# Kernel tuning notes

Hardware: AMD Instinct MI355X
Metric: run time of the kernel (lower is better)

The kernel has to match this reference:

```python
import jax, jax.numpy as jnp
import numpy as np
from jax import lax

B = 8; DIM = 256; NH = 8; PATCH = 8; WS = 28; STRIDE = 8; PAD = 14; ORF = 2.0; IMG = 448


def conv2d(x, w, stride, pad, groups=1):
    return lax.conv_general_dilated(
        x, w, (stride, stride), [(pad, pad), (pad, pad)],
        dimension_numbers=('NCHW', 'OIHW', 'NCHW'), feature_group_count=groups)


def ln_ch(x, g, b):
    # LayerNormProxy: LayerNorm over channel dim of NCHW
    m = jnp.mean(x, 1, keepdims=True)
    v = jnp.mean((x - m) ** 2, 1, keepdims=True)
    return (x - m) * lax.rsqrt(v + 1e-5) * g[None, :, None, None] + b[None, :, None, None]


def bilinear_sample(x, grid):
    # x: (N,C,H,W); grid: (N,Hg,Wg,2) in (x,y) order, [-1,1], align_corners=True, zeros padding
    N, C, H, W = x.shape
    gx = (grid[..., 0] + 1.0) * 0.5 * (W - 1)
    gy = (grid[..., 1] + 1.0) * 0.5 * (H - 1)
    x0 = jnp.floor(gx); y0 = jnp.floor(gy)
    x1 = x0 + 1.0; y1 = y0 + 1.0
    wx1 = gx - x0; wx0 = 1.0 - wx1
    wy1 = gy - y0; wy0 = 1.0 - wy1
    xf = x.reshape(N, C, H * W)

    def corner(ix, iy, w):
        valid = (ix >= 0) & (ix <= W - 1) & (iy >= 0) & (iy <= H - 1)
        ii = (jnp.clip(iy, 0, H - 1) * W + jnp.clip(ix, 0, W - 1)).astype(jnp.int32).reshape(N, -1)
        vals = jax.vmap(lambda f, i: f[:, i])(xf, ii)  # (N,C,Hg*Wg)
        return vals * (w * valid).reshape(N, 1, -1)

    out = (corner(x0, y0, wx0 * wy0) + corner(x1, y0, wx1 * wy0)
           + corner(x0, y1, wx0 * wy1) + corner(x1, y1, wx1 * wy1))
    return out.reshape(N, C, grid.shape[1], grid.shape[2])


def setup_inputs() -> dict:
    key = jax.random.key(0)
    ks = jax.random.split(key, 12)
    s = 0.02
    CG = 64
    return {
        'x': jax.random.normal(ks[0], (B, 3, IMG, IMG), jnp.float32),
        'patch_w': jax.random.normal(ks[1], (DIM, 3, PATCH, PATCH), jnp.float32) * s,
        'patch_b': jnp.zeros((DIM,), jnp.float32),
        'ln1_g': jnp.ones((DIM,), jnp.float32),
        'ln1_b': jnp.zeros((DIM,), jnp.float32),
        'wq': jax.random.normal(ks[2], (DIM, DIM), jnp.float32) * s,
        'bq': jnp.zeros((DIM,), jnp.float32),
        'wk': jax.random.normal(ks[3], (DIM, DIM), jnp.float32) * s,
        'bk': jnp.zeros((DIM,), jnp.float32),
        'wv': jax.random.normal(ks[4], (DIM, DIM), jnp.float32) * s,
        'bv': jnp.zeros((DIM,), jnp.float32),
        'wo': jax.random.normal(ks[5], (DIM, DIM), jnp.float32) * s,
        'bo': jnp.zeros((DIM,), jnp.float32),
        'off_dw_w': jax.random.normal(ks[6], (CG, 1, WS, WS), jnp.float32) * s,
        'off_dw_b': jnp.zeros((CG,), jnp.float32),
        'off_ln_g': jnp.ones((CG,), jnp.float32),
        'off_ln_b': jnp.zeros((CG,), jnp.float32),
        'off_pw_w': jax.random.normal(ks[7], (2, CG), jnp.float32) * s,
        'rpe_w1': jax.random.normal(ks[8], (32, 2), jnp.float32) * 0.1,
        'rpe_b1': jnp.zeros((32,), jnp.float32),
        'rpe_w2': jax.random.normal(ks[9], (2, 32), jnp.float32) * 0.1,
    }


def reference(x, patch_w, patch_b, ln1_g, ln1_b, wq, bq, wk, bk, wv, bv, wo, bo,
              off_dw_w, off_dw_b, off_ln_g, off_ln_b, off_pw_w, rpe_w1, rpe_b1, rpe_w2):
    Bn = x.shape[0]
    # patch embedding: Conv2d(3, dim, patch, patch) + LayerNormProxy
    feat = conv2d(x, patch_w, PATCH, 0) + patch_b[None, :, None, None]
    feat = ln_ch(feat, ln1_g, ln1_b)
    H, W = feat.shape[2], feat.shape[3]  # 56, 56
    G = (H // WS) * (W // WS)            # 4 groups
    CG = DIM // G; GH = NH // G; HC = DIM // NH
    # q projection (1x1 conv)
    q = jnp.einsum('oc,bchw->bohw', wq, feat) + bq[None, :, None, None]
    # offset network on per-group query features
    q_off = q.reshape(Bn * G, CG, H, W)
    off = conv2d(q_off, off_dw_w, STRIDE, PAD, groups=CG) + off_dw_b[None, :, None, None]
    off = jax.nn.gelu(ln_ch(off, off_ln_g, off_ln_b), approximate=False)
    off = jnp.einsum('oc,bchw->bohw', off_pw_w, off)   # (B*G, 2, Hk, Wk)
    Hk, Wk = off.shape[2], off.shape[3]
    ns = Hk * Wk
    rng = jnp.array([1.0 / (Hk - 1), 1.0 / (Wk - 1)], off.dtype).reshape(1, 2, 1, 1)
    offset = jnp.tanh(off) * rng * ORF
    offset = jnp.transpose(offset, (0, 2, 3, 1))  # (B*G, Hk, Wk, 2) in (y, x)
    # reference points, normalized to ~[-1, 1]
    ry = jnp.linspace(0.5, Hk - 0.5, Hk) / (Hk - 1) * 2.0 - 1.0
    rx = jnp.linspace(0.5, Wk - 0.5, Wk) / (Wk - 1) * 2.0 - 1.0
    ref = jnp.stack(jnp.meshgrid(ry, rx, indexing='ij'), -1)  # (Hk, Wk, 2)
    ref = jnp.broadcast_to(ref[None], (Bn * G, Hk, Wk, 2))
    pos = offset + ref
    # deformable sampling (grid expects (x, y) order)
    xs = bilinear_sample(feat.reshape(Bn * G, CG, H, W), pos[..., ::-1])  # (B*G, CG, Hk, Wk)
    xs = xs.reshape(Bn, DIM, ns)
    k = jnp.einsum('oc,bcn->bon', wk, xs) + bk[None, :, None]
    v = jnp.einsum('oc,bcn->bon', wv, xs) + bv[None, :, None]
    qh = q.reshape(Bn * NH, HC, H * W)
    kh = k.reshape(Bn * NH, HC, ns)
    vh = v.reshape(Bn * NH, HC, ns)
    attn = jnp.einsum('bcm,bcn->bmn', qh, kh) * (HC ** -0.5)  # (B*NH, HW, ns)
    # log-CPB relative position bias
    qy = jnp.linspace(0.0, float(H), H) / (H - 1) * 2.0 - 1.0
    qx = jnp.linspace(0.0, float(W), W) / (W - 1) * 2.0 - 1.0
    qg = jnp.stack(jnp.meshgrid(qy, qx, indexing='ij'), -1).reshape(H * W, 2)
    disp = (qg[None, :, None, :] - pos.reshape(Bn * G, ns, 2)[:, None, :, :]) * 4.0
    disp = jnp.sign(disp) * jnp.log2(jnp.abs(disp) + 1.0) / 3.0  # /log2(8)
    bias = jax.nn.relu(jnp.einsum('bmnc,hc->bmnh', disp, rpe_w1) + rpe_b1)
    bias = jnp.einsum('bmnh,oh->bmno', bias, rpe_w2)  # (B*G, HW, ns, GH)
    attn = attn + jnp.transpose(bias, (0, 3, 1, 2)).reshape(Bn * NH, H * W, ns)
    attn = jax.nn.softmax(attn, axis=-1)
    out = jnp.einsum('bmn,bcn->bcm', attn, vh).reshape(Bn, DIM, H, W)
    y = jnp.einsum('oc,bchw->bohw', wo, out) + bo[None, :, None, None]
    return (y, pos.reshape(Bn, G, Hk, Wk, 2), ref.reshape(Bn, G, Hk, Wk, 2))
```

## Files before the change

kernel.cpp:

```cpp
#include <hip/hip_runtime.h>
#include <cstddef>


typedef short bf16x8 __attribute__((ext_vector_type(8)));
typedef float f32x4 __attribute__((ext_vector_type(4)));

static __device__ __forceinline__ ushort f2bf(float f) {
  union { float f; unsigned u; } v; v.f = f;
  unsigned r = v.u + 0x7fffu + ((v.u >> 16) & 1u);
  return (ushort)(r >> 16);
}
static __device__ __forceinline__ float bf2f(ushort u) {
  union { unsigned u; float f; } v; v.u = ((unsigned)u) << 16;
  return v.f;
}

#define OFF_FEATB 0u
#define OFF_QPK   3211264u
#define OFF_Q     6422528u
#define OFF_POS   12845056u
#define OFF_XS    12849152u
#define OFF_KPK   12980224u
#define OFF_VPK   13045760u
#define OFF_PWP   13111296u
#define OFF_WQP   13135872u
#define OFF_WOP   13168640u
#define OFF_WKT   13201408u
#define OFF_WVT   13266944u

__global__ __launch_bounds__(256) void k_xcvt(
    const float* __restrict__ x, ushort* __restrict__ xb) {
  const size_t i0 = ((size_t)blockIdx.x * 256 + threadIdx.x) * 8;
  float4 v0 = *(const float4*)(x + i0);
  float4 v1 = *(const float4*)(x + i0 + 4);
  bf16x8 o;
  o[0] = (short)f2bf(v0.x); o[1] = (short)f2bf(v0.y);
  o[2] = (short)f2bf(v0.z); o[3] = (short)f2bf(v0.w);
  o[4] = (short)f2bf(v1.x); o[5] = (short)f2bf(v1.y);
  o[6] = (short)f2bf(v1.z); o[7] = (short)f2bf(v1.w);
  *(bf16x8*)(xb + i0) = o;
}

__global__ __launch_bounds__(256) void k_pack(
    const float* __restrict__ pw, const float* __restrict__ wq,
    const float* __restrict__ wk, const float* __restrict__ wv,
    const float* __restrict__ wo, ushort* __restrict__ pwp,
    ushort* __restrict__ wqp, ushort* __restrict__ wop,
    float* __restrict__ wkT, float* __restrict__ wvT) {
  const int o = blockIdx.x, t = threadIdx.x, m = blockIdx.y;
  if (m == 0) {
    if (t < 192) pwp[((t >> 3) * 256 + o) * 8 + (t & 7)] = f2bf(pw[o * 192 + t]);
  } else if (m == 1) {
    wqp[((t >> 3) * 256 + o) * 8 + (t & 7)] = f2bf(wq[o * 256 + t]);
  } else if (m == 2) {
    wop[((t >> 3) * 256 + o) * 8 + (t & 7)] = f2bf(wo[o * 256 + t]);
  } else if (m == 3) {
    wkT[t * 256 + o] = wk[o * 256 + t];
  } else {
    wvT[t * 256 + o] = wv[o * 256 + t];
  }
}

__global__ __launch_bounds__(256) void k_patch_mfma(
    const ushort* __restrict__ xb, const ushort* __restrict__ pwp,
    const float* __restrict__ pb, const float* __restrict__ g1,
    const float* __restrict__ b1, ushort* __restrict__ featb) {
  __shared__ ushort Bs[2][8192];
  const int t = threadIdx.x;
  const int lane = t & 63, w = t >> 6;
  const int lr = lane & 15, kg = lane >> 4;
  const int m_base = blockIdx.x * 128 + w * 32;

  size_t abase[2];
#pragma unroll
  for (int mr = 0; mr < 2; mr++) {
    int mA = m_base + mr * 16 + lr;
    int bA = mA / 3136;
    int posA = mA - bA * 3136;
    int ohA = posA / 56;
    int owA = posA - ohA * 56;
    abase[mr] = (((size_t)bA * 3) * 448 + ohA * 8) * 448 + owA * 8;
  }

  f32x4 acc[2][16];
#pragma unroll
  for (int f = 0; f < 16; f++) {
    float bv = pb[f * 16 + lr];
    acc[0][f] = (f32x4){bv, bv, bv, bv};
    acc[1][f] = (f32x4){bv, bv, bv, bv};
  }

  bf16x8 st[4];
#pragma unroll
  for (int i = 0; i < 4; i++)
    st[i] = *(const bf16x8*)(pwp + i * 2048 + t * 8);
#pragma unroll
  for (int i = 0; i < 4; i++)
    *(bf16x8*)(&Bs[0][i * 2048 + t * 8]) = st[i];
  __syncthreads();
  int p = 0;
  for (int ks = 0; ks < 6; ks++) {
    if (ks < 5) {
#pragma unroll
      for (int i = 0; i < 4; i++)
        st[i] = *(const bf16x8*)(pwp + (ks + 1) * 8192 + i * 2048 + t * 8);
    }
    const int k8 = ks * 4 + kg;
    const int ci = k8 >> 3, ii = k8 & 7;
    bf16x8 a0 = *(const bf16x8*)(xb + abase[0] + (size_t)ci * 200704 + ii * 448);
    bf16x8 a1 = *(const bf16x8*)(xb + abase[1] + (size_t)ci * 200704 + ii * 448);
    const ushort* bsl = &Bs[p][kg * 2048];
#pragma unroll
    for (int f = 0; f < 16; f++) {
      bf16x8 bfr = *(const bf16x8*)(bsl + (f * 16 + lr) * 8);
      acc[0][f] = __builtin_amdgcn_mfma_f32_16x16x32_bf16(a0, bfr, acc[0][f], 0, 0, 0);
      acc[1][f] = __builtin_amdgcn_mfma_f32_16x16x32_bf16(a1, bfr, acc[1][f], 0, 0, 0);
    }
    __syncthreads();
    if (ks < 5) {
#pragma unroll
      for (int i = 0; i < 4; i++)
        *(bf16x8*)(&Bs[p ^ 1][i * 2048 + t * 8]) = st[i];
      __syncthreads();
      p ^= 1;
    }
  }

#pragma unroll
  for (int mr = 0; mr < 2; mr++) {
    float mean[4], rstd[4];
#pragma unroll
    for (int j = 0; j < 4; j++) {
      float s1 = 0.f, s2 = 0.f;
#pragma unroll
      for (int f = 0; f < 16; f++) { float v = acc[mr][f][j]; s1 += v; s2 += v * v; }
#pragma unroll
      for (int off = 8; off >= 1; off >>= 1) {
        s1 += __shfl_xor(s1, off);
        s2 += __shfl_xor(s2, off);
      }
      float mn = s1 * (1.f / 256.f);
      float var = s2 * (1.f / 256.f) - mn * mn;
      mean[j] = mn; rstd[j] = rsqrtf(var + 1e-5f);
    }
#pragma unroll
    for (int f = 0; f < 16; f++) {
      const int c = f * 16 + lr;
      const float gg = g1[c], bb = b1[c];
#pragma unroll
      for (int j = 0; j < 4; j++) {
        const int mo = m_base + mr * 16 + kg * 4 + j;
        float v = (acc[mr][f][j] - mean[j]) * rstd[j] * gg + bb;
        featb[(size_t)mo * 256 + c] = f2bf(v);
      }
    }
  }
}

__global__ __launch_bounds__(256) void k_gemm_mfma(
    const ushort* __restrict__ apk, const ushort* __restrict__ wp,
    const float* __restrict__ bias, float* __restrict__ out,
    ushort* __restrict__ opk) {
  __shared__ float smem[16448];
  ushort* Bs = (ushort*)smem;
  float* sA = smem;
  const int t = threadIdx.x;
  const int lane = t & 63, w = t >> 6;
  const int lr = lane & 15, kg = lane >> 4;
  const int m_base = blockIdx.x * 128 + w * 32;

  f32x4 acc[2][16];
#pragma unroll
  for (int f = 0; f < 16; f++) {
    float bv = bias[f * 16 + lr];
    acc[0][f] = (f32x4){bv, bv, bv, bv};
    acc[1][f] = (f32x4){bv, bv, bv, bv};
  }
  const ushort* a0p = apk + (size_t)(m_base + lr) * 256;
  const ushort* a1p = a0p + 16 * 256;

  bf16x8 st[4];
#pragma unroll
  for (int i = 0; i < 4; i++) st[i] = *(const bf16x8*)(wp + i * 2048 + t * 8);
#pragma unroll
  for (int i = 0; i < 4; i++) *(bf16x8*)(Bs + i * 2048 + t * 8) = st[i];
  __syncthreads();
  int p = 0;
  for (int ks = 0; ks < 8; ks++) {
    if (ks < 7) {
#pragma unroll
      for (int i = 0; i < 4; i++)
        st[i] = *(const bf16x8*)(wp + (ks + 1) * 8192 + i * 2048 + t * 8);
    }
    bf16x8 a0 = *(const bf16x8*)(a0p + ks * 32 + kg * 8);
    bf16x8 a1 = *(const bf16x8*)(a1p + ks * 32 + kg * 8);
    const ushort* bsl = Bs + p * 8192 + kg * 2048;
#pragma unroll
    for (int f = 0; f < 16; f++) {
      bf16x8 bfr = *(const bf16x8*)(bsl + (f * 16 + lr) * 8);
      acc[0][f] = __builtin_amdgcn_mfma_f32_16x16x32_bf16(a0, bfr, acc[0][f], 0, 0, 0);
      acc[1][f] = __builtin_amdgcn_mfma_f32_16x16x32_bf16(a1, bfr, acc[1][f], 0, 0, 0);
    }
    __syncthreads();
    if (ks < 7) {
#pragma unroll
      for (int i = 0; i < 4; i++)
        *(bf16x8*)(Bs + (p ^ 1) * 8192 + i * 2048 + t * 8) = st[i];
      __syncthreads();
      p ^= 1;
    }
  }
  __syncthreads();

#pragma unroll
  for (int h = 0; h < 2; h++) {
    if ((w >> 1) == h) {
      const int loc0 = (w & 1) * 32;
#pragma unroll
      for (int mr = 0; mr < 2; mr++)
#pragma unroll
        for (int f = 0; f < 16; f++)
#pragma unroll
          for (int j = 0; j < 4; j++)
            sA[(loc0 + mr * 16 + kg * 4 + j) * 257 + f * 16 + lr] = acc[mr][f][j];
    }
    __syncthreads();
    const int R0 = blockIdx.x * 128 + h * 64;
    const int bh = R0 / 3136;
    const int pos0 = R0 % 3136;
    {
      const int c = t;
      float* op = out + ((size_t)bh * 256 + c) * 3136 + pos0;
#pragma unroll
      for (int i4 = 0; i4 < 16; i4++) {
        float4 v;
        v.x = sA[(i4 * 4 + 0) * 257 + c];
        v.y = sA[(i4 * 4 + 1) * 257 + c];
        v.z = sA[(i4 * 4 + 2) * 257 + c];
        v.w = sA[(i4 * 4 + 3) * 257 + c];
        *(float4*)(op + i4 * 4) = v;
      }
    }
    if (opk) {
      const int mm = t & 63, cs = t >> 6;
      const int c0 = cs * 64;
#pragma unroll
      for (int jj = 0; jj < 8; jj++) {
        bf16x8 v8;
#pragma unroll
        for (int e = 0; e < 8; e++)
          v8[e] = (short)f2bf(sA[mm * 257 + c0 + jj * 8 + e]);
        *(bf16x8*)(opk + (size_t)(R0 + mm) * 256 + c0 + jj * 8) = v8;
      }
    }
    __syncthreads();
  }
}

__global__ __launch_bounds__(128) void k_offset_conv(
    const float* __restrict__ q, const float* __restrict__ dww,
    float* __restrict__ convo) {
  const int bg = blockIdx.y;
  const int wv = threadIdx.x >> 6;
  const int lane = threadIdx.x & 63;
  const int ch = blockIdx.x * 2 + wv;
  const int b = bg >> 2, g = bg & 3;

  __shared__ float pl[2][7072];
  float* P = pl[wv];
  for (int idx = lane; idx < 7072; idx += 64) P[idx] = 0.f;

  const float* qb = q + ((size_t)b * 256 + g * 64 + ch) * 3136;
  if (lane < 56) {
    for (int r = 0; r < 56; r++) {
      int hr = r + 14;
      P[hr * 84 + (lane + 14) + (hr >> 3)] = qb[r * 56 + lane];
    }
  }
  const int oh = lane >> 3, ow = lane & 7;
  const int chs = __builtin_amdgcn_readfirstlane(ch);
  const float* wr = dww + (size_t)chs * 784;
  float acc = 0.f;
  const int r0 = oh * 8, c0 = ow * 8;
  for (int i = 0; i < 28; i++) {
    int hr = r0 + i;
    const float* prow = P + hr * 84 + c0 + (hr >> 3);
    const float* wrr = wr + i * 28;
#pragma unroll
    for (int j = 0; j < 28; j++)
      acc = fmaf(prow[j], wrr[j], acc);
  }
  convo[bg * 4096 + lane * 64 + ch] = acc;
}

__global__ __launch_bounds__(256) void k_offset_post(
    const float* __restrict__ convo, const float* __restrict__ dwb,
    const float* __restrict__ lng, const float* __restrict__ lnb,
    const float* __restrict__ pww, float* __restrict__ pos_ws,
    float* __restrict__ out_pos, float* __restrict__ out_ref) {
  const int bg = blockIdx.y;
  const int wv = threadIdx.x >> 6;
  const int lane = threadIdx.x & 63;
  const int idx = blockIdx.x * 4 + wv;
  const int oh = idx >> 3, ow = idx & 7;

  float acc = convo[bg * 4096 + idx * 64 + lane] + dwb[lane];

  float s1 = acc, s2 = acc * acc;
#pragma unroll
  for (int off = 32; off >= 1; off >>= 1) {
    s1 += __shfl_xor(s1, off);
    s2 += __shfl_xor(s2, off);
  }
  float m = s1 * (1.f / 64.f);
  float var = s2 * (1.f / 64.f) - m * m;
  float val = (acc - m) * rsqrtf(var + 1e-5f) * lng[lane] + lnb[lane];
  val = 0.5f * val * (1.f + erff(val * 0.70710678118654752f));
  float p0 = pww[lane] * val, p1 = pww[64 + lane] * val;
#pragma unroll
  for (int off = 32; off >= 1; off >>= 1) {
    p0 += __shfl_xor(p0, off);
    p1 += __shfl_xor(p1, off);
  }
  if (lane == 0) {
    float offy = tanhf(p0) * (2.0f / 7.0f);
    float offx = tanhf(p1) * (2.0f / 7.0f);
    float ry = (0.5f + oh) * (2.0f / 7.0f) - 1.0f;
    float rx = (0.5f + ow) * (2.0f / 7.0f) - 1.0f;
    float py = offy + ry, px = offx + rx;
    int o = bg * 128 + idx * 2;
    pos_ws[o] = py;  pos_ws[o + 1] = px;
    out_pos[o] = py; out_pos[o + 1] = px;
    out_ref[o] = ry; out_ref[o + 1] = rx;
  }
}

__global__ __launch_bounds__(256) void k_sample_kv(
    const ushort* __restrict__ featb, const float* __restrict__ pos_ws,
    const float* __restrict__ wkT, const float* __restrict__ bk,
    const float* __restrict__ wvT, const float* __restrict__ bv,
    ushort* __restrict__ kpk, ushort* __restrict__ vpk) {
  const int b = blockIdx.y;
  const int n = blockIdx.x;
  const int t = threadIdx.x;
  const int g = t >> 6, lane = t & 63;
  const int bg = b * 4 + g;

  __shared__ float sxs[256];
  {
    float py = pos_ws[bg * 128 + n * 2];
    float px = pos_ws[bg * 128 + n * 2 + 1];
    float gx = (px + 1.f) * 27.5f;
    float gy = (py + 1.f) * 27.5f;
    float x0f = floorf(gx), y0f = floorf(gy);
    int x0 = (int)x0f, y0 = (int)y0f;
    float wx1 = gx - x0f, wx0 = 1.f - wx1;
    float wy1 = gy - y0f, wy0 = 1.f - wy1;
    const size_t mb = (size_t)b * 3136;
    const int cofs = g * 64 + lane;
    float acc = 0.f;
    if (x0 >= 0 && x0 <= 55 && y0 >= 0 && y0 <= 55)
      acc = fmaf(bf2f(featb[(mb + y0 * 56 + x0) * 256 + cofs]), wx0 * wy0, acc);
    if (x0 + 1 >= 0 && x0 + 1 <= 55 && y0 >= 0 && y0 <= 55)
      acc = fmaf(bf2f(featb[(mb + y0 * 56 + x0 + 1) * 256 + cofs]), wx1 * wy0, acc);
    if (x0 >= 0 && x0 <= 55 && y0 + 1 >= 0 && y0 + 1 <= 55)
      acc = fmaf(bf2f(featb[(mb + (y0 + 1) * 56 + x0) * 256 + cofs]), wx0 * wy1, acc);
    if (x0 + 1 >= 0 && x0 + 1 <= 55 && y0 + 1 >= 0 && y0 + 1 <= 55)
      acc = fmaf(bf2f(featb[(mb + (y0 + 1) * 56 + x0 + 1) * 256 + cofs]), wx1 * wy1, acc);
    sxs[g * 64 + lane] = acc;
  }
  __syncthreads();

  float ak = bk[t], av = bv[t];
  for (int c = 0; c < 256; c++) {
    float xv = sxs[c];
    ak = fmaf(wkT[c * 256 + t], xv, ak);
    av = fmaf(wvT[c * 256 + t], xv, av);
  }
  const int h = t >> 5, cc = t & 31;
  const size_t base = (size_t)(b * 8 + h) * 2048;
  kpk[base + (size_t)((cc >> 3) * 64 + n) * 8 + (cc & 7)] = f2bf(ak);
  vpk[base + (size_t)((n >> 3) * 32 + cc) * 8 + (n & 7)] = f2bf(av);
}

__global__ __launch_bounds__(256) void k_attn_mfma(
    const ushort* __restrict__ qpk, const ushort* __restrict__ kpk,
    const ushort* __restrict__ vpk, const float* __restrict__ pos_ws,
    const float* __restrict__ w1, const float* __restrict__ b1,
    const float* __restrict__ w2, ushort* __restrict__ attnpk) {
  const int bg = blockIdx.y;
  const int b = bg >> 2, g = bg & 3;
  const int m0 = blockIdx.x * 64;
  const int t = threadIdx.x;
  const int lane = t & 63, w = t >> 6;
  const int lr = lane & 15, kg = lane >> 4;

  __shared__ ushort Pbuf[4][16 * 88];
  __shared__ ushort outb[64 * 72];
  __shared__ float posl[128];
  __shared__ float4 rpe4[32];
  __shared__ float rpeB[32];

  if (t < 128) posl[t] = pos_ws[bg * 128 + t];
  if (t < 32) {
    rpe4[t] = make_float4(w1[t * 2], w1[t * 2 + 1], b1[t], w2[t]);
    rpeB[t] = w2[32 + t];
  }
  __syncthreads();

  float qgy[4], qgx[4];
#pragma unroll
  for (int j = 0; j < 4; j++) {
    int m = m0 + w * 16 + kg * 4 + j;
    int my = m / 56, mx = m % 56;
    qgy[j] = (float)my * (56.0f / 55.0f) * (2.0f / 55.0f) - 1.0f;
    qgx[j] = (float)mx * (56.0f / 55.0f) * (2.0f / 55.0f) - 1.0f;
  }
  float tyv[16], txv[16];
#pragma unroll
  for (int nf = 0; nf < 4; nf++) {
    int n = nf * 16 + lr;
    float py = posl[2 * n], px = posl[2 * n + 1];
#pragma unroll
    for (int j = 0; j < 4; j++) {
      float dy = (qgy[j] - py) * 4.f;
      float dx = (qgx[j] - px) * 4.f;
      tyv[nf * 4 + j] = copysignf(__log2f(fabsf(dy) + 1.f) * (1.f / 3.f), dy);
      txv[nf * 4 + j] = copysignf(__log2f(fabsf(dx) + 1.f) * (1.f / 3.f), dx);
    }
  }
  float bb0[16], bb1[16];
#pragma unroll
  for (int p = 0; p < 16; p++) { bb0[p] = 0.f; bb1[p] = 0.f; }
  for (int jj = 0; jj < 32; jj++) {
    float4 r = rpe4[jj];
    float wb = rpeB[jj];
#pragma unroll
    for (int p = 0; p < 16; p++) {
      float hv = fmaxf(fmaf(r.x, tyv[p], fmaf(r.y, txv[p], r.z)), 0.f);
      bb0[p] = fmaf(r.w, hv, bb0[p]);
      bb1[p] = fmaf(wb, hv, bb1[p]);
    }
  }

  const int mrow = m0 + w * 16 + lr;
  const float scale = 0.17677669529663687f;
  ushort* pb = Pbuf[w];

  f32x4 oacc[2][2];
#pragma unroll
  for (int gh = 0; gh < 2; gh++)
#pragma unroll
    for (int cf = 0; cf < 2; cf++) oacc[gh][cf] = (f32x4){0.f, 0.f, 0.f, 0.f};

#pragma unroll
  for (int gh = 0; gh < 2; gh++) {
    bf16x8 a = *(const bf16x8*)(qpk +
        ((size_t)(b * 3136 + mrow) * 256 + g * 64 + gh * 32 + kg * 8));
    const ushort* kbase = kpk + (size_t)(b * 8 + g * 2 + gh) * 2048;
    f32x4 s[4];
#pragma unroll
    for (int nf = 0; nf < 4; nf++) {
      bf16x8 bfr = *(const bf16x8*)(kbase + (size_t)(kg * 64 + nf * 16 + lr) * 8);
      s[nf] = __builtin_amdgcn_mfma_f32_16x16x32_bf16(
          a, bfr, (f32x4){0.f, 0.f, 0.f, 0.f}, 0, 0, 0);
    }
#pragma unroll
    for (int nf = 0; nf < 4; nf++)
#pragma unroll
      for (int j = 0; j < 4; j++)
        s[nf][j] = fmaf(s[nf][j], scale,
                        gh ? bb1[nf * 4 + j] : bb0[nf * 4 + j]);
#pragma unroll
    for (int j = 0; j < 4; j++) {
      float m1 = fmaxf(fmaxf(s[0][j], s[1][j]), fmaxf(s[2][j], s[3][j]));
#pragma unroll
      for (int o = 8; o >= 1; o >>= 1) m1 = fmaxf(m1, __shfl_xor(m1, o));
      float ss = 0.f;
#pragma unroll
      for (int nf = 0; nf < 4; nf++) {
        float e = __expf(s[nf][j] - m1);
        s[nf][j] = e;
        ss += e;
      }
#pragma unroll
      for (int o = 8; o >= 1; o >>= 1) ss += __shfl_xor(ss, o);
      float inv = 1.f / ss;
#pragma unroll
      for (int nf = 0; nf < 4; nf++) s[nf][j] *= inv;
    }
#pragma unroll
    for (int nf = 0; nf < 4; nf++)
#pragma unroll
      for (int j = 0; j < 4; j++)
        pb[(kg * 4 + j) * 88 + nf * 16 + lr] = f2bf(s[nf][j]);
    const ushort* vbase = vpk + (size_t)(b * 8 + g * 2 + gh) * 2048;
#pragma unroll
    for (int ks = 0; ks < 2; ks++) {
      bf16x8 pa = *(const bf16x8*)(pb + lr * 88 + ks * 32 + kg * 8);
#pragma unroll
      for (int cf = 0; cf < 2; cf++) {
        bf16x8 vb = *(const bf16x8*)(vbase +
            (size_t)((ks * 4 + kg) * 32 + cf * 16 + lr) * 8);
        oacc[gh][cf] = __builtin_amdgcn_mfma_f32_16x16x32_bf16(
            pa, vb, oacc[gh][cf], 0, 0, 0);
      }
    }
  }

#pragma unroll
  for (int gh = 0; gh < 2; gh++)
#pragma unroll
    for (int cf = 0; cf < 2; cf++)
#pragma unroll
      for (int j = 0; j < 4; j++)
        outb[(w * 16 + kg * 4 + j) * 72 + gh * 32 + cf * 16 + lr] =
            f2bf(oacc[gh][cf][j]);
  __syncthreads();
#pragma unroll
  for (int r2 = 0; r2 < 2; r2++) {
    int row = (t >> 3) + r2 * 32;
    int chunk = t & 7;
    bf16x8 v8 = *(const bf16x8*)(outb + row * 72 + chunk * 8);
    *(bf16x8*)(attnpk +
               ((size_t)(b * 3136 + m0 + row) * 256 + g * 64 + chunk * 8)) = v8;
  }
}

extern "C" void kernel_launch(void* const* d_in, const int* in_sizes, int n_in,
                              void* d_out, int out_size, void* d_ws,
                              size_t ws_size, hipStream_t stream) {
  const float* x       = (const float*)d_in[0];
  const float* patch_w = (const float*)d_in[1];
  const float* patch_b = (const float*)d_in[2];
  const float* ln1_g   = (const float*)d_in[3];
  const float* ln1_b   = (const float*)d_in[4];
  const float* wq      = (const float*)d_in[5];
  const float* bq      = (const float*)d_in[6];
  const float* wk      = (const float*)d_in[7];
  const float* bk      = (const float*)d_in[8];
  const float* wv      = (const float*)d_in[9];
  const float* bv      = (const float*)d_in[10];
  const float* wo      = (const float*)d_in[11];
  const float* bo      = (const float*)d_in[12];
  const float* off_dw_w = (const float*)d_in[13];
  const float* off_dw_b = (const float*)d_in[14];
  const float* off_ln_g = (const float*)d_in[15];
  const float* off_ln_b = (const float*)d_in[16];
  const float* off_pw_w = (const float*)d_in[17];
  const float* rpe_w1  = (const float*)d_in[18];
  const float* rpe_b1  = (const float*)d_in[19];
  const float* rpe_w2  = (const float*)d_in[20];

  float* ws = (float*)d_ws;
  ushort* featb = (ushort*)(ws + OFF_FEATB);
  ushort* attnpk = featb;
  ushort* qpk = (ushort*)(ws + OFF_QPK);
  float* q    = ws + OFF_Q;
  ushort* xb  = (ushort*)(ws + OFF_Q);
  float* posw = ws + OFF_POS;
  float* convo = ws + OFF_XS;
  ushort* kpk = (ushort*)(ws + OFF_KPK);
  ushort* vpk = (ushort*)(ws + OFF_VPK);
  ushort* pwp = (ushort*)(ws + OFF_PWP);
  ushort* wqp = (ushort*)(ws + OFF_WQP);
  ushort* wop = (ushort*)(ws + OFF_WOP);
  float* wkT  = ws + OFF_WKT;
  float* wvT  = ws + OFF_WVT;

  float* y = (float*)d_out;
  float* out_pos = y + 6422528;
  float* out_ref = out_pos + 4096;

  hipLaunchKernelGGL(k_xcvt, dim3(2352), dim3(256), 0, stream, x, xb);
  hipLaunchKernelGGL(k_pack, dim3(256, 5), dim3(256), 0, stream,
                     patch_w, wq, wk, wv, wo, pwp, wqp, wop, wkT, wvT);
  hipLaunchKernelGGL(k_patch_mfma, dim3(196), dim3(256), 0, stream,
                     xb, pwp, patch_b, ln1_g, ln1_b, featb);
  hipLaunchKernelGGL(k_gemm_mfma, dim3(196), dim3(256), 0, stream,
                     featb, wqp, bq, q, qpk);
  hipLaunchKernelGGL(k_offset_conv, dim3(32, 32), dim3(128), 0, stream,
                     q, off_dw_w, convo);
  hipLaunchKernelGGL(k_offset_post, dim3(16, 32), dim3(256), 0, stream,
                     convo, off_dw_b, off_ln_g, off_ln_b, off_pw_w,
                     posw, out_pos, out_ref);
  hipLaunchKernelGGL(k_sample_kv, dim3(64, 8), dim3(256), 0, stream,
                     featb, posw, wkT, bk, wvT, bv, kpk, vpk);
  hipLaunchKernelGGL(k_attn_mfma, dim3(49, 32), dim3(256), 0, stream,
                     qpk, kpk, vpk, posw, rpe_w1, rpe_b1, rpe_w2, attnpk);
  hipLaunchKernelGGL(k_gemm_mfma, dim3(196), dim3(256), 0, stream,
                     attnpk, wop, bo, y, (ushort*)nullptr);
}
```

Baseline: 249.7 us.

## Fuse input bf16 conversion into patch GEMM, batch K/V samples, fp16 RPE MLP

Drops the separate fp32-to-bf16 conversion kernel for the input image and converts x on the fly inside the patch-embedding MFMA kernel, so the extra launch and intermediate buffer round trip go away. The K/V sampling kernel now handles four sample points per block, which lets each wkT/wvT weight load serve four FMAs and cuts the grid by four. The per-element relative-position-bias MLP in attention now runs in packed fp16 math to double ALU throughput. The trade-off is lower precision in the bias computation, where fp16 accumulation across 32 hidden units could lose accuracy, and fewer blocks (occupancy) in sample_kv.

```diff
diff --git a/kernel.cpp b/kernel.cpp
--- a/kernel.cpp
+++ b/kernel.cpp
@@ -4,6 +4,7 @@
 
 typedef short bf16x8 __attribute__((ext_vector_type(8)));
 typedef float f32x4 __attribute__((ext_vector_type(4)));
+typedef _Float16 h2v __attribute__((ext_vector_type(2)));
 
 static __device__ __forceinline__ ushort f2bf(float f) {
   union { float f; unsigned u; } v; v.f = f;
@@ -27,19 +28,6 @@
 #define OFF_WOP   13168640u
 #define OFF_WKT   13201408u
 #define OFF_WVT   13266944u
-
-__global__ __launch_bounds__(256) void k_xcvt(
-    const float* __restrict__ x, ushort* __restrict__ xb) {
-  const size_t i0 = ((size_t)blockIdx.x * 256 + threadIdx.x) * 8;
-  float4 v0 = *(const float4*)(x + i0);
-  float4 v1 = *(const float4*)(x + i0 + 4);
-  bf16x8 o;
-  o[0] = (short)f2bf(v0.x); o[1] = (short)f2bf(v0.y);
-  o[2] = (short)f2bf(v0.z); o[3] = (short)f2bf(v0.w);
-  o[4] = (short)f2bf(v1.x); o[5] = (short)f2bf(v1.y);
-  o[6] = (short)f2bf(v1.z); o[7] = (short)f2bf(v1.w);
-  *(bf16x8*)(xb + i0) = o;
-}
 
 __global__ __launch_bounds__(256) void k_pack(
     const float* __restrict__ pw, const float* __restrict__ wq,
@@ -62,7 +50,7 @@
 }
 
 __global__ __launch_bounds__(256) void k_patch_mfma(
-    const ushort* __restrict__ xb, const ushort* __restrict__ pwp,
+    const float* __restrict__ x, const ushort* __restrict__ pwp,
     const float* __restrict__ pb, const float* __restrict__ g1,
     const float* __restrict__ b1, ushort* __restrict__ featb) {
   __shared__ ushort Bs[2][8192];
@@ -107,8 +95,19 @@
     }
     const int k8 = ks * 4 + kg;
     const int ci = k8 >> 3, ii = k8 & 7;
-    bf16x8 a0 = *(const bf16x8*)(xb + abase[0] + (size_t)ci * 200704 + ii * 448);
-    bf16x8 a1 = *(const bf16x8*)(xb + abase[1] + (size_t)ci * 200704 + ii * 448);
+    bf16x8 a0, a1;
+#pragma unroll
+    for (int mr = 0; mr < 2; mr++) {
+      const float* xp = x + abase[mr] + (size_t)ci * 200704 + ii * 448;
+      float4 v0 = *(const float4*)xp;
+      float4 v1 = *(const float4*)(xp + 4);
+      bf16x8 a;
+      a[0] = (short)f2bf(v0.x); a[1] = (short)f2bf(v0.y);
+      a[2] = (short)f2bf(v0.z); a[3] = (short)f2bf(v0.w);
+      a[4] = (short)f2bf(v1.x); a[5] = (short)f2bf(v1.y);
+      a[6] = (short)f2bf(v1.z); a[7] = (short)f2bf(v1.w);
+      if (mr == 0) a0 = a; else a1 = a;
+    }
     const ushort* bsl = &Bs[p][kg * 2048];
 #pragma unroll
     for (int f = 0; f < 16; f++) {
@@ -341,46 +340,63 @@
     const float* __restrict__ wvT, const float* __restrict__ bv,
     ushort* __restrict__ kpk, ushort* __restrict__ vpk) {
   const int b = blockIdx.y;
-  const int n = blockIdx.x;
+  const int n0 = blockIdx.x * 4;
   const int t = threadIdx.x;
   const int g = t >> 6, lane = t & 63;
   const int bg = b * 4 + g;
 
-  __shared__ float sxs[256];
+  __shared__ float sxs[256 * 4];
   {
-    float py = pos_ws[bg * 128 + n * 2];
-    float px = pos_ws[bg * 128 + n * 2 + 1];
-    float gx = (px + 1.f) * 27.5f;
-    float gy = (py + 1.f) * 27.5f;
-    float x0f = floorf(gx), y0f = floorf(gy);
-    int x0 = (int)x0f, y0 = (int)y0f;
-    float wx1 = gx - x0f, wx0 = 1.f - wx1;
-    float wy1 = gy - y0f, wy0 = 1.f - wy1;
     const size_t mb = (size_t)b * 3136;
     const int cofs = g * 64 + lane;
-    float acc = 0.f;
-    if (x0 >= 0 && x0 <= 55 && y0 >= 0 && y0 <= 55)
-      acc = fmaf(bf2f(featb[(mb + y0 * 56 + x0) * 256 + cofs]), wx0 * wy0, acc);
-    if (x0 + 1 >= 0 && x0 + 1 <= 55 && y0 >= 0 && y0 <= 55)
-      acc = fmaf(bf2f(featb[(mb + y0 * 56 + x0 + 1) * 256 + cofs]), wx1 * wy0, acc);
-    if (x0 >= 0 && x0 <= 55 && y0 + 1 >= 0 && y0 + 1 <= 55)
-      acc = fmaf(bf2f(featb[(mb + (y0 + 1) * 56 + x0) * 256 + cofs]), wx0 * wy1, acc);
-    if (x0 + 1 >= 0 && x0 + 1 <= 55 && y0 + 1 >= 0 && y0 + 1 <= 55)
-      acc = fmaf(bf2f(featb[(mb + (y0 + 1) * 56 + x0 + 1) * 256 + cofs]), wx1 * wy1, acc);
-    sxs[g * 64 + lane] = acc;
+    float av4[4];
+#pragma unroll
+    for (int u = 0; u < 4; u++) {
+      const int n = n0 + u;
+      float py = pos_ws[bg * 128 + n * 2];
+      float px = pos_ws[bg * 128 + n * 2 + 1];
+      float gx = (px + 1.f) * 27.5f;
+      float gy = (py + 1.f) * 27.5f;
+      float x0f = floorf(gx), y0f = floorf(gy);
+      int x0 = (int)x0f, y0 = (int)y0f;
+      float wx1 = gx - x0f, wx0 = 1.f - wx1;
+      float wy1 = gy - y0f, wy0 = 1.f - wy1;
+      float acc = 0.f;
+      if (x0 >= 0 && x0 <= 55 && y0 >= 0 && y0 <= 55)
+        acc = fmaf(bf2f(featb[(mb + y0 * 56 + x0) * 256 + cofs]), wx0 * wy0, acc);
+      if (x0 + 1 >= 0 && x0 + 1 <= 55 && y0 >= 0 && y0 <= 55)
+        acc = fmaf(bf2f(featb[(mb + y0 * 56 + x0 + 1) * 256 + cofs]), wx1 * wy0, acc);
+      if (x0 >= 0 && x0 <= 55 && y0 + 1 >= 0 && y0 + 1 <= 55)
+        acc = fmaf(bf2f(featb[(mb + (y0 + 1) * 56 + x0) * 256 + cofs]), wx0 * wy1, acc);
+      if (x0 + 1 >= 0 && x0 + 1 <= 55 && y0 + 1 >= 0 && y0 + 1 <= 55)
+        acc = fmaf(bf2f(featb[(mb + (y0 + 1) * 56 + x0 + 1) * 256 + cofs]), wx1 * wy1, acc);
+      av4[u] = acc;
+    }
+    *(float4*)&sxs[(g * 64 + lane) * 4] =
+        make_float4(av4[0], av4[1], av4[2], av4[3]);
   }
   __syncthreads();
 
-  float ak = bk[t], av = bv[t];
+  float ak[4], av[4];
+#pragma unroll
+  for (int u = 0; u < 4; u++) { ak[u] = bk[t]; av[u] = bv[t]; }
   for (int c = 0; c < 256; c++) {
-    float xv = sxs[c];
-    ak = fmaf(wkT[c * 256 + t], xv, ak);
-    av = fmaf(wvT[c * 256 + t], xv, av);
+    float wkv = wkT[c * 256 + t];
+    float wvv = wvT[c * 256 + t];
+    float4 xv = *(const float4*)&sxs[c * 4];
+    ak[0] = fmaf(wkv, xv.x, ak[0]); av[0] = fmaf(wvv, xv.x, av[0]);
+    ak[1] = fmaf(wkv, xv.y, ak[1]); av[1] = fmaf(wvv, xv.y, av[1]);
+    ak[2] = fmaf(wkv, xv.z, ak[2]); av[2] = fmaf(wvv, xv.z, av[2]);
+    ak[3] = fmaf(wkv, xv.w, ak[3]); av[3] = fmaf(wvv, xv.w, av[3]);
   }
   const int h = t >> 5, cc = t & 31;
   const size_t base = (size_t)(b * 8 + h) * 2048;
-  kpk[base + (size_t)((cc >> 3) * 64 + n) * 8 + (cc & 7)] = f2bf(ak);
-  vpk[base + (size_t)((n >> 3) * 32 + cc) * 8 + (n & 7)] = f2bf(av);
+#pragma unroll
+  for (int u = 0; u < 4; u++) {
+    const int n = n0 + u;
+    kpk[base + (size_t)((cc >> 3) * 64 + n) * 8 + (cc & 7)] = f2bf(ak[u]);
+    vpk[base + (size_t)((n >> 3) * 32 + cc) * 8 + (n & 7)] = f2bf(av[u]);
+  }
 }
 
 __global__ __launch_bounds__(256) void k_attn_mfma(
@@ -398,13 +414,20 @@
   __shared__ ushort Pbuf[4][16 * 88];
   __shared__ ushort outb[64 * 72];
   __shared__ float posl[128];
-  __shared__ float4 rpe4[32];
-  __shared__ float rpeB[32];
+  __shared__ h2v rpeh[32][5];
 
   if (t < 128) posl[t] = pos_ws[bg * 128 + t];
   if (t < 32) {
-    rpe4[t] = make_float4(w1[t * 2], w1[t * 2 + 1], b1[t], w2[t]);
-    rpeB[t] = w2[32 + t];
+    _Float16 a0 = (_Float16)w1[t * 2];
+    _Float16 a1 = (_Float16)w1[t * 2 + 1];
+    _Float16 a2 = (_Float16)b1[t];
+    _Float16 a3 = (_Float16)w2[t];
+    _Float16 a4 = (_Float16)w2[32 + t];
+    rpeh[t][0] = (h2v){a0, a0};
+    rpeh[t][1] = (h2v){a1, a1};
+    rpeh[t][2] = (h2v){a2, a2};
+    rpeh[t][3] = (h2v){a3, a3};
+    rpeh[t][4] = (h2v){a4, a4};
   }
   __syncthreads();
 
@@ -429,18 +452,32 @@
       txv[nf * 4 + j] = copysignf(__log2f(fabsf(dx) + 1.f) * (1.f / 3.f), dx);
     }
   }
+  h2v ty2[8], tx2[8], bb02[8], bb12[8];
+  const h2v zz = (h2v){(_Float16)0.f, (_Float16)0.f};
+#pragma unroll
+  for (int k = 0; k < 8; k++) {
+    ty2[k] = (h2v){(_Float16)tyv[2 * k], (_Float16)tyv[2 * k + 1]};
+    tx2[k] = (h2v){(_Float16)txv[2 * k], (_Float16)txv[2 * k + 1]};
+    bb02[k] = zz; bb12[k] = zz;
+  }
+  for (int jj = 0; jj < 32; jj++) {
+    h2v hy = rpeh[jj][0], hx = rpeh[jj][1], hb = rpeh[jj][2];
+    h2v ha = rpeh[jj][3], hc = rpeh[jj][4];
+#pragma unroll
+    for (int k = 0; k < 8; k++) {
+      h2v hv = hy * ty2[k] + (hx * tx2[k] + hb);
+      hv = __builtin_elementwise_max(hv, zz);
+      bb02[k] = bb02[k] + ha * hv;
+      bb12[k] = bb12[k] + hc * hv;
+    }
+  }
   float bb0[16], bb1[16];
 #pragma unroll
-  for (int p = 0; p < 16; p++) { bb0[p] = 0.f; bb1[p] = 0.f; }
-  for (int jj = 0; jj < 32; jj++) {
-    float4 r = rpe4[jj];
-    float wb = rpeB[jj];
-#pragma unroll
-    for (int p = 0; p < 16; p++) {
-      float hv = fmaxf(fmaf(r.x, tyv[p], fmaf(r.y, txv[p], r.z)), 0.f);
-      bb0[p] = fmaf(r.w, hv, bb0[p]);
-      bb1[p] = fmaf(wb, hv, bb1[p]);
-    }
+  for (int k = 0; k < 8; k++) {
+    bb0[2 * k]     = (float)bb02[k].x;
+    bb0[2 * k + 1] = (float)bb02[k].y;
+    bb1[2 * k]     = (float)bb12[k].x;
+    bb1[2 * k + 1] = (float)bb12[k].y;
   }
 
   const int mrow = m0 + w * 16 + lr;
@@ -557,7 +594,6 @@
   ushort* attnpk = featb;
   ushort* qpk = (ushort*)(ws + OFF_QPK);
   float* q    = ws + OFF_Q;
-  ushort* xb  = (ushort*)(ws + OFF_Q);
   float* posw = ws + OFF_POS;
   float* convo = ws + OFF_XS;
   ushort* kpk = (ushort*)(ws + OFF_KPK);
@@ -572,11 +608,10 @@
   float* out_pos = y + 6422528;
   float* out_ref = out_pos + 4096;
 
-  hipLaunchKernelGGL(k_xcvt, dim3(2352), dim3(256), 0, stream, x, xb);
   hipLaunchKernelGGL(k_pack, dim3(256, 5), dim3(256), 0, stream,
                      patch_w, wq, wk, wv, wo, pwp, wqp, wop, wkT, wvT);
   hipLaunchKernelGGL(k_patch_mfma, dim3(196), dim3(256), 0, stream,
-                     xb, pwp, patch_b, ln1_g, ln1_b, featb);
+                     x, pwp, patch_b, ln1_g, ln1_b, featb);
   hipLaunchKernelGGL(k_gemm_mfma, dim3(196), dim3(256), 0, stream,
                      featb, wqp, bq, q, qpk);
   hipLaunchKernelGGL(k_offset_conv, dim3(32, 32), dim3(128), 0, stream,
@@ -584,7 +619,7 @@
   hipLaunchKernelGGL(k_offset_post, dim3(16, 32), dim3(256), 0, stream,
                      convo, off_dw_b, off_ln_g, off_ln_b, off_pw_w,
                      posw, out_pos, out_ref);
-  hipLaunchKernelGGL(k_sample_kv, dim3(64, 8), dim3(256), 0, stream,
+  hipLaunchKernelGGL(k_sample_kv, dim3(16, 8), dim3(256), 0, stream,
                      featb, posw, wkT, bk, wvT, bv, kpk, vpk);
   hipLaunchKernelGGL(k_attn_mfma, dim3(49, 32), dim3(256), 0, stream,
                      qpk, kpk, vpk, posw, rpe_w1, rpe_b1, rpe_w2, attnpk);
```

After: 246.7 us. About the same (-1.2%).
